# Kernel optimization log

Measured on AMD Instinct MI355X. Metric: run time of the kernel, lower is better.

The kernel has to match this reference:

```python
import jax, jax.numpy as jnp
import numpy as np
from jax.scipy.special import logsumexp

VOCAB = 50000; CHAR_VOCAB = 100
B, S, LC = 32, 256, 16
WDIM, CDIM, CNN_OUT, POS, ENR = 256, 124, 32, 36, 7
H = 512
T = 18  # num_classes + 1
IN0 = WDIM + POS + CNN_OUT + ENR  # 331
IN1 = 2 * H


def setup_inputs() -> dict:
    ks = jax.random.split(jax.random.key(0), 40)
    p = lambda i, shape: jax.random.normal(ks[i], shape, jnp.float32) * 0.05
    inp = {
        "x_word": jax.random.randint(ks[0], (B, S), 0, VOCAB),
        "x_pos": jax.random.normal(ks[1], (B, S, POS), jnp.float32),
        "x_char": jax.random.randint(ks[2], (B, S, LC), 0, CHAR_VOCAB),
        "x_enrich": jax.random.normal(ks[3], (B, S, ENR), jnp.float32),
        "mask": jnp.ones((B, S), jnp.bool_),
        "y_word": jax.random.randint(ks[4], (B, S), 0, T),
        "word_embed_W": p(5, (VOCAB, WDIM)),
        "char_embed_W": p(6, (CHAR_VOCAB, CDIM)),
        "cnn_W": p(7, (CNN_OUT, CDIM, 5)),
        "cnn_b": p(8, (CNN_OUT,)),
        "lin1_W": p(9, (128, IN1)), "lin1_b": p(10, (128,)),
        "lin2_W": p(11, (T, 128)), "lin2_b": p(12, (T,)),
        "crf_start": p(13, (T,)), "crf_end": p(14, (T,)), "crf_trans": p(15, (T, T)),
    }
    for j, (nm, din) in enumerate([("l0f", IN0), ("l0b", IN0), ("l1f", IN1), ("l1b", IN1)]):
        inp[nm + "_Wih"] = p(16 + 3 * j, (4 * H, din))
        inp[nm + "_Whh"] = p(17 + 3 * j, (4 * H, H))
        inp[nm + "_b"] = p(18 + 3 * j, (4 * H,))
    return inp


def _lstm_dir(xT, Wih, Whh, b, reverse):
    # xT: [S, B, D]; PyTorch gate order i, f, g, o; bias = b_ih + b_hh folded.
    Bn, Hn = xT.shape[1], Whh.shape[1]
    def step(carry, xt):
        h, c = carry
        z = xt @ Wih.T + h @ Whh.T + b
        i, f, g, o = jnp.split(z, 4, axis=-1)
        c2 = jax.nn.sigmoid(f) * c + jax.nn.sigmoid(i) * jnp.tanh(g)
        h2 = jax.nn.sigmoid(o) * jnp.tanh(c2)
        return (h2, c2), h2
    z0 = jnp.zeros((Bn, Hn), xT.dtype)
    _, hs = jax.lax.scan(step, (z0, z0), xT, reverse=reverse)
    return hs  # [S, B, H]


def _bilstm(x, prm):
    # x: [B, S, D]; prm: 4 tuples (Wih, Whh, b) = layer0 fwd/bwd, layer1 fwd/bwd
    xT = jnp.swapaxes(x, 0, 1)
    h = jnp.concatenate([_lstm_dir(xT, *prm[0], False), _lstm_dir(xT, *prm[1], True)], -1)
    h = jnp.concatenate([_lstm_dir(h, *prm[2], False), _lstm_dir(h, *prm[3], True)], -1)
    return jnp.swapaxes(h, 0, 1)  # [B, S, 2H]


def _emissions(x_word, x_pos, x_char, x_enrich, word_embed_W, char_embed_W,
               cnn_W, cnn_b, prm, lin1_W, lin1_b, lin2_W, lin2_b):
    Bn, Sn = x_word.shape
    we = word_embed_W[x_word]                               # [B, S, WDIM]
    ce = char_embed_W[x_char]                               # [B, S, LC, CDIM]
    ce = ce.reshape(Bn * Sn, LC, CDIM).transpose(0, 2, 1)   # [B*S, CDIM, LC]
    conv = jax.lax.conv_general_dilated(
        ce, cnn_W, (1,), 'VALID', dimension_numbers=('NCH', 'OIH', 'NCH')
    ) + cnn_b[None, :, None]                                # [B*S, CNN_OUT, LC-4]
    cpool = conv.max(-1).reshape(Bn, Sn, CNN_OUT)           # global max pool
    x = jax.nn.relu(jnp.concatenate([we, x_pos, cpool, x_enrich], -1))  # [B, S, 331]
    h = _bilstm(x, prm)                                     # [B, S, 1024]
    h1 = h @ lin1_W.T + lin1_b                              # [B, S, 128] (no activation)
    return h1 @ lin2_W.T + lin2_b                           # [B, S, T]


def _crf_nll(em, tags, mask, start, end, trans):
    # pytorch-crf: -llh with reduction='token_mean'
    m = mask.astype(em.dtype)
    em_sc = jnp.take_along_axis(em, tags[..., None], 2)[..., 0]        # [B, S]
    tr_sc = trans[tags[:, :-1], tags[:, 1:]]                           # [B, S-1]
    num = start[tags[:, 0]] + em_sc[:, 0] + jnp.sum(m[:, 1:] * (tr_sc + em_sc[:, 1:]), 1)
    seq_len = mask.sum(1).astype(jnp.int32)
    last_tag = jnp.take_along_axis(tags, (seq_len - 1)[:, None], 1)[:, 0]
    num = num + end[last_tag]
    score = start[None] + em[:, 0]                                     # [B, T]
    def step(sc, inp):
        e_t, m_t = inp
        nxt = logsumexp(sc[:, :, None] + trans[None] + e_t[:, None, :], axis=1)
        return jnp.where(m_t[:, None], nxt, sc), None
    score, _ = jax.lax.scan(step, score,
                            (jnp.swapaxes(em[:, 1:], 0, 1), jnp.swapaxes(mask[:, 1:], 0, 1)))
    logZ = logsumexp(score + end[None], -1)
    return -(num - logZ).sum() / m.sum()


def _viterbi(em, start, end, trans):
    # decode() is called without mask -> all timesteps valid
    score = start[None] + em[:, 0]                                     # [B, T]
    def step(sc, e_t):
        cand = sc[:, :, None] + trans[None]                            # [B, T, T]
        return jnp.max(cand, 1) + e_t, jnp.argmax(cand, 1)
    score, hist = jax.lax.scan(step, score, jnp.swapaxes(em[:, 1:], 0, 1))  # hist: [S-1, B, T]
    last = jnp.argmax(score + end[None], -1)                           # [B]
    def back(tag, idx_t):
        prev = jnp.take_along_axis(idx_t, tag[:, None], 1)[:, 0]
        return prev, prev
    _, prevs = jax.lax.scan(back, last, hist, reverse=True)            # [S-1, B]
    return jnp.concatenate([prevs, last[None]], 0).T                   # [B, S]


def reference(x_word, x_pos, x_char, x_enrich, mask, y_word,
              word_embed_W, char_embed_W, cnn_W, cnn_b,
              lin1_W, lin1_b, lin2_W, lin2_b,
              crf_start, crf_end, crf_trans,
              l0f_Wih, l0f_Whh, l0f_b, l0b_Wih, l0b_Whh, l0b_b,
              l1f_Wih, l1f_Whh, l1f_b, l1b_Wih, l1b_Whh, l1b_b):
    prm = [(l0f_Wih, l0f_Whh, l0f_b), (l0b_Wih, l0b_Whh, l0b_b),
           (l1f_Wih, l1f_Whh, l1f_b), (l1b_Wih, l1b_Whh, l1b_b)]
    em = _emissions(x_word, x_pos, x_char, x_enrich, word_embed_W, char_embed_W,
                    cnn_W, cnn_b, prm, lin1_W, lin1_b, lin2_W, lin2_b)
    decoded = _viterbi(em, crf_start, crf_end, crf_trans)
    loss = _crf_nll(em, y_word, mask, crf_start, crf_end, crf_trans)
    return em, decoded, loss
```

## Files before the change

kernel.cpp:

```cpp
#include <hip/hip_runtime.h>
#include <hip/hip_bf16.h>
#include <math.h>

constexpr int NB   = 32;
constexpr int NS   = 256;
constexpr int NLC  = 16;
constexpr int NWD  = 256;
constexpr int NCD  = 124;
constexpr int NCO  = 32;
constexpr int NPOS = 36;
constexpr int NENR = 7;
constexpr int NH   = 512;
constexpr int NT   = 18;
constexpr int NIN0 = 331;
constexpr int NIN0P= 352;
constexpr int NIN1 = 1024;
constexpr int NBS  = NB*NS;
constexpr int NG4  = 4*NH;
constexpr int NGS  = 4096;
constexpr int NHID = 128;
constexpr int NCHUNK = 16;

typedef __attribute__((ext_vector_type(8))) short short8v;
typedef __attribute__((ext_vector_type(4))) float f32x4;
typedef __attribute__((address_space(3))) unsigned lds_u32;
typedef __attribute__((address_space(1))) const unsigned glb_u32;

__device__ __forceinline__ float sigmoidf_(float x){ return 1.0f/(1.0f+expf(-x)); }
__device__ __forceinline__ short f2bf(float f) {
    union { __hip_bfloat16 h; short s; } u;
    u.h = __float2bfloat16(f);
    return u.s;
}
__device__ __forceinline__ float bf2f(short s) {
    union { unsigned u; float f; } v;
    v.u = ((unsigned)(unsigned short)s) << 16;
    return v.f;
}
__device__ __forceinline__ unsigned packbf3(float v) {
    short hi = f2bf(v);
    short lo = f2bf(v - bf2f(hi));
    return ((unsigned)(unsigned short)hi << 16) | (unsigned short)lo;
}
__device__ __forceinline__ void unpack8(const unsigned* w, short8v& hi, short8v& lo) {
    union U { short8v s; unsigned u[4]; } H, L;
    #pragma unroll
    for (int i = 0; i < 4; i++) {
        H.u[i] = (w[2*i+1] & 0xFFFF0000u) | (w[2*i] >> 16);
        L.u[i] = (w[2*i+1] << 16) | (w[2*i] & 0xFFFFu);
    }
    hi = H.s; lo = L.s;
}
__device__ __forceinline__ unsigned ld_sc1(const unsigned* p) {
    return __hip_atomic_load(p, __ATOMIC_RELAXED, __HIP_MEMORY_SCOPE_AGENT);
}
__device__ __forceinline__ void st_sc1(unsigned* p, unsigned v) {
    __hip_atomic_store(p, v, __ATOMIC_RELAXED, __HIP_MEMORY_SCOPE_AGENT);
}

__global__ __launch_bounds__(128) void k_features(const int* __restrict__ x_word,
    const float* __restrict__ x_pos, const int* __restrict__ x_char,
    const float* __restrict__ x_enr, const float* __restrict__ wembW,
    const float* __restrict__ cembW, const float* __restrict__ cnnW,
    const float* __restrict__ cnnb,
    unsigned short* __restrict__ xh, unsigned short* __restrict__ xl)
{
    __shared__ float ce[NLC][NCD];
    __shared__ float wT[310*33];
    __shared__ float cv[NCO][14];
    __shared__ float cpool[NCO];
    int n = blockIdx.x;
    int tid = threadIdx.x;
    for (int i = tid; i < NLC*NCD; i += 128) {
        int l = i / NCD, c = i % NCD;
        ce[l][c] = cembW[x_char[n*NLC + l]*NCD + c];
    }
    float acc3[3] = {0.f, 0.f, 0.f};
    #pragma unroll
    for (int half = 0; half < 2; half++) {
        int csta = half*62;
        __syncthreads();
        for (int i = tid; i < 310*32; i += 128) {
            int o = i / 310, ck = i - o*310;
            wT[ck*33 + o] = cnnW[o*(NCD*5) + csta*5 + ck];
        }
        __syncthreads();
        #pragma unroll
        for (int q = 0; q < 3; q++) {
            int p = tid + q*128;
            int o = p & 31, t = p >> 5;
            float acc = acc3[q];
            for (int c = 0; c < 62; c++) {
                #pragma unroll
                for (int k = 0; k < 5; k++)
                    acc += ce[t+k][csta + c] * wT[(c*5+k)*33 + o];
            }
            acc3[q] = acc;
        }
    }
    #pragma unroll
    for (int q = 0; q < 3; q++) {
        int p = tid + q*128;
        cv[p & 31][p >> 5] = acc3[q];
    }
    __syncthreads();
    if (tid < NCO) {
        float m = cv[tid][0];
        #pragma unroll
        for (int t = 1; t < 12; t++) m = fmaxf(m, cv[tid][t]);
        cpool[tid] = m + cnnb[tid];
    }
    __syncthreads();
    int widx = x_word[n];
    for (int j = tid; j < NIN0P; j += 128) {
        float v;
        if (j < NWD)            v = wembW[(size_t)widx*NWD + j];
        else if (j < NWD+NPOS)  v = x_pos[n*NPOS + (j-NWD)];
        else if (j < NWD+NPOS+NCO) v = cpool[j-(NWD+NPOS)];
        else if (j < NIN0)      v = x_enr[n*NENR + (j-(NWD+NPOS+NCO))];
        else                    v = 0.f;
        v = fmaxf(v, 0.f);
        short hi = f2bf(v);
        xh[(size_t)n*NIN0P + j] = (unsigned short)hi;
        xl[(size_t)n*NIN0P + j] = (unsigned short)f2bf(v - bf2f(hi));
    }
}

__global__ void k_pack_w(const float* __restrict__ W,
                         unsigned short* __restrict__ Wh, unsigned short* __restrict__ Wl,
                         int N, int Ksrc, int Kdst)
{
    int idx = blockIdx.x*256 + threadIdx.x;
    if (idx >= N*Kdst) return;
    int n = idx / Kdst, k = idx % Kdst;
    float v = (k < Ksrc) ? W[(size_t)n*Ksrc + k] : 0.f;
    short hi = f2bf(v);
    Wh[idx] = (unsigned short)hi;
    Wl[idx] = (unsigned short)f2bf(v - bf2f(hi));
}

constexpr int HBK = 32;
__global__ __launch_bounds__(256, 2) void k_gemm_hl(
    const unsigned short* __restrict__ Ah, const unsigned short* __restrict__ Al,
    const unsigned short* __restrict__ Bh, const unsigned short* __restrict__ Bl,
    const float* __restrict__ bias, float* __restrict__ C,
    int M, int N, int K)
{
    __shared__ unsigned short sA[2][2][128*HBK];
    __shared__ unsigned short sB[2][2][128*HBK];
    int bx = blockIdx.x, by = blockIdx.y;
    {
        int nMb = gridDim.x, nNb = gridDim.y;
        if (((nMb | nNb) & 3) == 0) {
            int lin = by * nMb + bx;
            int sid = lin >> 4, rem = lin & 15;
            int spr = nNb >> 2;
            int sm = sid / spr, sn = sid - sm*spr;
            bx = sm*4 + (rem >> 2);
            by = sn*4 + (rem & 3);
        }
    }
    int bm = bx*128, bn = by*128;
    int tid = threadIdx.x;
    int l = tid & 63, wv = tid >> 6;
    int wm = wv >> 1, wn = wv & 1;
    int lr = l & 15, lk = l >> 4;

    const unsigned short* gplane = (wv == 0) ? Ah : (wv == 1) ? Al : (wv == 2) ? Bh : Bl;
    int gbase = (wv < 2) ? bm : bn;
    unsigned short* lplane0 = (wv == 0) ? sA[0][0] : (wv == 1) ? sA[0][1]
                           : (wv == 2) ? sB[0][0] : sB[0][1];
    unsigned short* lplane1 = (wv == 0) ? sA[1][0] : (wv == 1) ? sA[1][1]
                           : (wv == 2) ? sB[1][0] : sB[1][1];
    int lrow = l >> 2;
    int gu = (l & 3);

    auto stage = [&](int kt, int buf) {
        unsigned short* lp0 = buf ? lplane1 : lplane0;
        #pragma unroll
        for (int rr = 0; rr < 8; rr++) {
            int row = rr*16 + lrow;
            int guS = gu ^ (row & 3);
            glb_u32* gp = (glb_u32*)(gplane + (size_t)(gbase + row)*K + (size_t)kt*HBK + guS*8);
            lds_u32* lp = (lds_u32*)(lp0 + (rr*16)*HBK);
            __builtin_amdgcn_global_load_lds(gp, lp, 16, 0, 0);
        }
    };

    f32x4 acc[4][4];
    #pragma unroll
    for (int i = 0; i < 4; i++)
        #pragma unroll
        for (int j = 0; j < 4; j++) acc[i][j] = (f32x4){0.f,0.f,0.f,0.f};

    int KT = K / HBK;
    stage(0, 0);
    int cur = 0;
    for (int kt = 0; kt < KT; kt++) {
        __syncthreads();
        if (kt+1 < KT) stage(kt+1, cur^1);
        short8v fAh[4], fAl[4], fBh[4], fBl[4];
        #pragma unroll
        for (int f = 0; f < 4; f++) {
            int ra = wm*64 + f*16 + lr, ua = (lk ^ (ra & 3))*8;
            fAh[f] = *(const short8v*)&sA[cur][0][ra*HBK + ua];
            fAl[f] = *(const short8v*)&sA[cur][1][ra*HBK + ua];
            int rb = wn*64 + f*16 + lr, ub = (lk ^ (rb & 3))*8;
            fBh[f] = *(const short8v*)&sB[cur][0][rb*HBK + ub];
            fBl[f] = *(const short8v*)&sB[cur][1][rb*HBK + ub];
        }
        #pragma unroll
        for (int i = 0; i < 4; i++)
            #pragma unroll
            for (int j = 0; j < 4; j++) {
                acc[i][j] = __builtin_amdgcn_mfma_f32_16x16x32_bf16(fAh[i], fBh[j], acc[i][j], 0, 0, 0);
                acc[i][j] = __builtin_amdgcn_mfma_f32_16x16x32_bf16(fAl[i], fBh[j], acc[i][j], 0, 0, 0);
                acc[i][j] = __builtin_amdgcn_mfma_f32_16x16x32_bf16(fAh[i], fBl[j], acc[i][j], 0, 0, 0);
            }
        cur ^= 1;
    }
    #pragma unroll
    for (int i = 0; i < 4; i++) {
        int m0 = bm + wm*64 + i*16 + lk*4;
        #pragma unroll
        for (int j = 0; j < 4; j++) {
            int n0 = bn + wn*64 + j*16 + lr;
            float bv = bias[n0];
            #pragma unroll
            for (int q = 0; q < 4; q++)
                C[(size_t)(m0+q)*N + n0] = acc[i][j][q] + bv;
        }
    }
}

__global__ __launch_bounds__(512, 2) void k_lstm_layer(
    const float* __restrict__ zxcat,
    const float* __restrict__ Whh_f, const float* __restrict__ Whh_b,
    unsigned short* __restrict__ h_hi, unsigned short* __restrict__ h_lo,
    unsigned* __restrict__ hbf, unsigned* __restrict__ flags)
{
    int chunk = blockIdx.x;
    int dir   = blockIdx.y;
    int tid = threadIdx.x;
    int wv = tid >> 6, l = tid & 63;
    int g  = wv & 3;
    int ks = wv >> 2;
    int lr = l & 15, lk = l >> 4;
    const float* zx  = zxcat + dir*NG4;
    const float* Whh = dir ? Whh_b : Whh_f;
    unsigned* hb = hbf + (size_t)dir * (2*NB*NH);
    unsigned* flag = flags + (size_t)dir * NCHUNK * 16;

    short8v bwh[2][8], bwl[2][8];
    #pragma unroll
    for (int uh = 0; uh < 2; uh++) {
        const float* wrow = Whh + ((size_t)(g*NH + chunk*32 + uh*16 + lr))*NH + ks*256 + lk*8;
        #pragma unroll
        for (int kt = 0; kt < 8; kt++) {
            float u[8];
            *(float4*)&u[0] = *(const float4*)(wrow + kt*32);
            *(float4*)&u[4] = *(const float4*)(wrow + kt*32 + 4);
            short8v sh, sl;
            #pragma unroll
            for (int j = 0; j < 8; j++) {
                short hi = f2bf(u[j]);
                sh[j] = hi;
                sl[j] = f2bf(u[j] - bf2f(hi));
            }
            bwh[uh][kt] = sh; bwl[uh][kt] = sl;
        }
    }

    __shared__ unsigned hstage[32*516];
    __shared__ float zsh[2][4][32][33];
    float c0 = 0.f, c1 = 0.f;

    for (int t = 0; t < NS; t++) {
        int t_eff = dir ? (NS-1-t) : t;

        float pz[2][4];
        #pragma unroll
        for (int cc = 0; cc < 2; cc++) {
            int cell = tid + cc*512, b = cell >> 5, u = cell & 31;
            const float* zr = zx + ((size_t)(b*NS + t_eff))*NGS + chunk*32 + u;
            #pragma unroll
            for (int g2 = 0; g2 < 4; g2++) pz[cc][g2] = zr[g2*NH];
        }

        if (t > 0) {
            {
                const unsigned* fp = &flag[(l & 15)*16];
                unsigned v;
                do { v = ld_sc1(fp); } while (!__all((int)(v >= (unsigned)t)));
                asm volatile("" ::: "memory");
            }
            const unsigned* hp = hb + ((t-1)&1)*(NB*NH);
            unsigned sv[32];
            #pragma unroll
            for (int i = 0; i < 32; i++) sv[i] = ld_sc1(hp + i*512 + tid);
            #pragma unroll
            for (int i = 0; i < 32; i++) hstage[i*516 + tid] = sv[i];
        }
        __syncthreads();

        f32x4 acc[2][2][3];
        #pragma unroll
        for (int bh = 0; bh < 2; bh++)
            #pragma unroll
            for (int uh = 0; uh < 2; uh++)
                #pragma unroll
                for (int q = 0; q < 3; q++) acc[bh][uh][q] = (f32x4){0.f,0.f,0.f,0.f};
        if (t > 0) {
            #pragma unroll
            for (int kt = 0; kt < 8; kt++) {
                short8v ah[2], al[2];
                #pragma unroll
                for (int bh = 0; bh < 2; bh++) {
                    unsigned w8[8];
                    const unsigned* sp = hstage + (bh*16+lr)*516 + ks*256 + kt*32 + lk*8;
                    *(uint4*)&w8[0] = *(const uint4*)sp;
                    *(uint4*)&w8[4] = *(const uint4*)(sp+4);
                    unpack8(w8, ah[bh], al[bh]);
                }
                #pragma unroll
                for (int bh = 0; bh < 2; bh++)
                    #pragma unroll
                    for (int uh = 0; uh < 2; uh++) {
                        acc[bh][uh][0] = __builtin_amdgcn_mfma_f32_16x16x32_bf16(ah[bh], bwh[uh][kt], acc[bh][uh][0], 0, 0, 0);
                        acc[bh][uh][1] = __builtin_amdgcn_mfma_f32_16x16x32_bf16(al[bh], bwh[uh][kt], acc[bh][uh][1], 0, 0, 0);
                        acc[bh][uh][2] = __builtin_amdgcn_mfma_f32_16x16x32_bf16(ah[bh], bwl[uh][kt], acc[bh][uh][2], 0, 0, 0);
                    }
            }
        }
        #pragma unroll
        for (int bh = 0; bh < 2; bh++)
            #pragma unroll
            for (int uh = 0; uh < 2; uh++)
                #pragma unroll
                for (int j = 0; j < 4; j++)
                    zsh[ks][g][bh*16 + lk*4 + j][uh*16 + lr] =
                        acc[bh][uh][0][j] + acc[bh][uh][1][j] + acc[bh][uh][2][j];
        __syncthreads();

        unsigned hq0 = 0, hq1 = 0;
        #pragma unroll
        for (int cc = 0; cc < 2; cc++) {
            int cell = tid + cc*512, b = cell >> 5, u = cell & 31;
            float zi = pz[cc][0] + zsh[0][0][b][u] + zsh[1][0][b][u];
            float zf = pz[cc][1] + zsh[0][1][b][u] + zsh[1][1][b][u];
            float zg = pz[cc][2] + zsh[0][2][b][u] + zsh[1][2][b][u];
            float zo = pz[cc][3] + zsh[0][3][b][u] + zsh[1][3][b][u];
            float cold = cc ? c1 : c0;
            float cn = sigmoidf_(zf)*cold + sigmoidf_(zi)*tanhf(zg);
            float hn = sigmoidf_(zo)*tanhf(cn);
            unsigned pk = packbf3(hn);
            if (cc) { c1 = cn; hq1 = pk; } else { c0 = cn; hq0 = pk; }
            st_sc1(&hb[(size_t)(t&1)*(NB*NH) + b*NH + chunk*32 + u], pk);
        }
        __syncthreads();
        if (tid == 0)
            st_sc1(&flag[chunk*16], (unsigned)(t+1));
        #pragma unroll
        for (int cc = 0; cc < 2; cc++) {
            int cell = tid + cc*512, b = cell >> 5, u = cell & 31;
            unsigned pk = cc ? hq1 : hq0;
            size_t o = ((size_t)(b*NS + t_eff))*NIN1 + dir*NH + chunk*32 + u;
            h_hi[o] = (unsigned short)(pk >> 16);
            h_lo[o] = (unsigned short)(pk & 0xFFFFu);
        }
    }
}

__global__ __launch_bounds__(256) void k_lin2(const float* __restrict__ hid,
    const float* __restrict__ W2, const float* __restrict__ b2, float* __restrict__ em)
{
    int flat = blockIdx.x*256 + threadIdx.x;
    if (flat >= NBS*NT) return;
    int m = flat / NT, j = flat % NT;
    const float* hr = hid + (size_t)m*NHID;
    const float* wr = W2 + j*NHID;
    float acc = b2[j];
    #pragma unroll 8
    for (int k = 0; k < NHID; k += 4) {
        float4 h4 = *(const float4*)(hr+k);
        float4 w4 = *(const float4*)(wr+k);
        acc += h4.x*w4.x + h4.y*w4.y + h4.z*w4.z + h4.w*w4.w;
    }
    em[flat] = acc;
}

__global__ __launch_bounds__(64) void k_crf(const float* __restrict__ em,
    const int* __restrict__ tags, const float* __restrict__ start,
    const float* __restrict__ endv, const float* __restrict__ trans,
    float* __restrict__ dec, float* __restrict__ partial)
{
    __shared__ float tr[NT][NT];
    __shared__ float vsc[NT], nsc[NT];
    __shared__ unsigned char hist[NS][NT];
    __shared__ float numsh;
    int b = blockIdx.x, tid = threadIdx.x;
    for (int i = tid; i < NT*NT; i += 64) tr[i/NT][i%NT] = trans[i];
    if (tid < NT) {
        float e0 = em[((size_t)b*NS)*NT + tid];
        vsc[tid] = start[tid] + e0;
        nsc[tid] = start[tid] + e0;
    }
    __syncthreads();
    const int* tg = tags + b*NS;
    float num = 0.f;
    for (int t = 1; t < NS; t++) {
        float nv_v = 0.f, nv_n = 0.f;
        if (tid < NT) {
            float emv = em[((size_t)b*NS + t)*NT + tid];
            float best = -1e30f; int bi = 0;
            float m = -1e30f;
            for (int i = 0; i < NT; i++) {
                float v = vsc[i] + tr[i][tid];
                if (v > best) { best = v; bi = i; }
                m = fmaxf(m, nsc[i] + tr[i][tid]);
            }
            hist[t][tid] = (unsigned char)bi;
            nv_v = best + emv;
            float s = 0.f;
            for (int i = 0; i < NT; i++) s += expf(nsc[i] + tr[i][tid] - m);
            nv_n = m + logf(s) + emv;
        } else if (tid == 32) {
            num += tr[tg[t-1]][tg[t]] + em[((size_t)b*NS + t)*NT + tg[t]];
        }
        __syncthreads();
        if (tid < NT) { vsc[tid] = nv_v; nsc[tid] = nv_n; }
        __syncthreads();
    }
    if (tid == 32) numsh = num;
    __syncthreads();
    if (tid == 0) {
        float bv = vsc[0] + endv[0]; int tag = 0;
        for (int j = 1; j < NT; j++) { float v = vsc[j] + endv[j]; if (v > bv) { bv = v; tag = j; } }
        dec[b*NS + NS-1] = (float)tag;
        for (int t = NS-1; t >= 1; t--) { tag = hist[t][tag]; dec[b*NS + t-1] = (float)tag; }
        float m = -1e30f;
        for (int j = 0; j < NT; j++) m = fmaxf(m, nsc[j] + endv[j]);
        float s = 0.f;
        for (int j = 0; j < NT; j++) s += expf(nsc[j] + endv[j] - m);
        float logZ = m + logf(s);
        float numer = start[tg[0]] + em[((size_t)b*NS)*NT + tg[0]] + numsh + endv[tg[NS-1]];
        partial[b] = -(numer - logZ);
    }
}

__global__ void k_loss_final(const float* __restrict__ partial, float* __restrict__ loss)
{
    if (threadIdx.x == 0 && blockIdx.x == 0) {
        float s = 0.f;
        for (int b = 0; b < NB; b++) s += partial[b];
        *loss = s / (float)(NB*NS);
    }
}

extern "C" void kernel_launch(void* const* d_in, const int* in_sizes, int n_in,
                              void* d_out, int out_size, void* d_ws, size_t ws_size,
                              hipStream_t stream)
{
    const int*   x_word = (const int*)d_in[0];
    const float* x_pos  = (const float*)d_in[1];
    const int*   x_char = (const int*)d_in[2];
    const float* x_enr  = (const float*)d_in[3];
    const int*   y_word = (const int*)d_in[5];
    const float* wembW  = (const float*)d_in[6];
    const float* cembW  = (const float*)d_in[7];
    const float* cnnW   = (const float*)d_in[8];
    const float* cnnb   = (const float*)d_in[9];
    const float* lin1W  = (const float*)d_in[10];
    const float* lin1b  = (const float*)d_in[11];
    const float* lin2W  = (const float*)d_in[12];
    const float* lin2b  = (const float*)d_in[13];
    const float* crf_s  = (const float*)d_in[14];
    const float* crf_e  = (const float*)d_in[15];
    const float* crf_tr = (const float*)d_in[16];
    const float* l0f_Wih = (const float*)d_in[17];
    const float* l0f_Whh = (const float*)d_in[18];
    const float* l0f_b   = (const float*)d_in[19];
    const float* l0b_Wih = (const float*)d_in[20];
    const float* l0b_Whh = (const float*)d_in[21];
    const float* l0b_b   = (const float*)d_in[22];
    const float* l1f_Wih = (const float*)d_in[23];
    const float* l1f_Whh = (const float*)d_in[24];
    const float* l1f_b   = (const float*)d_in[25];
    const float* l1b_Wih = (const float*)d_in[26];
    const float* l1b_Whh = (const float*)d_in[27];
    const float* l1b_b   = (const float*)d_in[28];

    char* wsb = (char*)d_ws;
    size_t off = 0;
    auto alloc = [&](size_t bytes) { char* p = wsb + off; off += (bytes + 255) & ~(size_t)255; return p; };
    unsigned short* xh  = (unsigned short*)alloc((size_t)NBS*NIN0P*2);
    unsigned short* xl  = (unsigned short*)alloc((size_t)NBS*NIN0P*2);
    unsigned short* w0h = (unsigned short*)alloc((size_t)NGS*NIN0P*2);
    unsigned short* w0l = (unsigned short*)alloc((size_t)NGS*NIN0P*2);
    unsigned short* w1h = (unsigned short*)alloc((size_t)NGS*NIN1*2);
    unsigned short* w1l = (unsigned short*)alloc((size_t)NGS*NIN1*2);
    unsigned short* wlh = (unsigned short*)alloc((size_t)NHID*NIN1*2);
    unsigned short* wll = (unsigned short*)alloc((size_t)NHID*NIN1*2);
    float*    zxcat = (float*)alloc((size_t)NBS*NGS*4);
    unsigned short* h0h = (unsigned short*)alloc((size_t)NBS*NIN1*2);
    unsigned short* h0l = (unsigned short*)alloc((size_t)NBS*NIN1*2);
    unsigned short* h1h = (unsigned short*)alloc((size_t)NBS*NIN1*2);
    unsigned short* h1l = (unsigned short*)alloc((size_t)NBS*NIN1*2);
    float*    hid1  = (float*)alloc((size_t)NBS*NHID*4);
    float*    partial = (float*)alloc(256);
    float*    bias0 = (float*)alloc((size_t)NGS*4);
    float*    bias1 = (float*)alloc((size_t)NGS*4);
    unsigned* hbf   = (unsigned*)alloc((size_t)2*2*NB*NH*4);
    unsigned* flags = (unsigned*)alloc((size_t)2*NCHUNK*16*4);

    float* em_out   = (float*)d_out;
    float* dec_out  = em_out + (size_t)NBS*NT;
    float* loss_out = dec_out + NBS;

    k_pack_w<<<(NG4*NIN0P+255)/256, 256, 0, stream>>>(l0f_Wih, w0h, w0l, NG4, NIN0, NIN0P);
    k_pack_w<<<(NG4*NIN0P+255)/256, 256, 0, stream>>>(l0b_Wih, w0h + (size_t)NG4*NIN0P, w0l + (size_t)NG4*NIN0P, NG4, NIN0, NIN0P);
    k_pack_w<<<(NG4*NIN1+255)/256, 256, 0, stream>>>(l1f_Wih, w1h, w1l, NG4, NIN1, NIN1);
    k_pack_w<<<(NG4*NIN1+255)/256, 256, 0, stream>>>(l1b_Wih, w1h + (size_t)NG4*NIN1, w1l + (size_t)NG4*NIN1, NG4, NIN1, NIN1);
    k_pack_w<<<(NHID*NIN1+255)/256, 256, 0, stream>>>(lin1W, wlh, wll, NHID, NIN1, NIN1);
    hipMemcpyAsync(bias0,       l0f_b, NG4*4, hipMemcpyDeviceToDevice, stream);
    hipMemcpyAsync(bias0 + NG4, l0b_b, NG4*4, hipMemcpyDeviceToDevice, stream);
    hipMemcpyAsync(bias1,       l1f_b, NG4*4, hipMemcpyDeviceToDevice, stream);
    hipMemcpyAsync(bias1 + NG4, l1b_b, NG4*4, hipMemcpyDeviceToDevice, stream);
    k_features<<<NBS, 128, 0, stream>>>(x_word, x_pos, x_char, x_enr, wembW, cembW, cnnW, cnnb, xh, xl);
    k_gemm_hl<<<dim3(NBS/128, NGS/128), 256, 0, stream>>>(xh, xl, w0h, w0l, bias0, zxcat, NBS, NGS, NIN0P);
    hipMemsetAsync(flags, 0, (size_t)2*NCHUNK*16*4, stream);
    k_lstm_layer<<<dim3(NCHUNK, 2), 512, 0, stream>>>(zxcat, l0f_Whh, l0b_Whh, h0h, h0l, hbf, flags);
    k_gemm_hl<<<dim3(NBS/128, NGS/128), 256, 0, stream>>>(h0h, h0l, w1h, w1l, bias1, zxcat, NBS, NGS, NIN1);
    hipMemsetAsync(flags, 0, (size_t)2*NCHUNK*16*4, stream);
    k_lstm_layer<<<dim3(NCHUNK, 2), 512, 0, stream>>>(zxcat, l1f_Whh, l1b_Whh, h1h, h1l, hbf, flags);
    k_gemm_hl<<<dim3(NBS/128, NHID/128), 256, 0, stream>>>(h1h, h1l, wlh, wll, lin1b, hid1, NBS, NHID, NIN1);
    k_lin2<<<(NBS*NT+255)/256, 256, 0, stream>>>(hid1, lin2W, lin2b, em_out);
    k_crf<<<NB, 64, 0, stream>>>(em_out, y_word, crf_s, crf_e, crf_tr, dec_out, partial);
    k_loss_final<<<1, 64, 0, stream>>>(partial, loss_out);
}
```

Measured before the change: 3.611 ms.

## Per-wave flags in LSTM recurrence, fuse head GEMMs, merge weight packing

Each wave in the LSTM recurrence now publishes its own progress flag after waiting only on its own outstanding stores, replacing the block-wide barrier before a single flag store. Consumers poll the per-wave flags with 64-bit loads. The lin1 GEMM and lin2 projection are fused into one kernel that keeps the hidden activations in LDS, and the five weight-packing launches become one. This cuts per-timestep synchronization latency and a few launches. It adds polling traffic and relies on the vmcnt wait to order the h stores before the flag.

```diff
diff --git a/kernel.cpp b/kernel.cpp
--- a/kernel.cpp
+++ b/kernel.cpp
@@ -21,6 +21,11 @@
 constexpr int NHID = 128;
 constexpr int NCHUNK = 16;
 
+constexpr int SW0 = NG4*NIN0P;
+constexpr int SW1 = NG4*NIN1;
+constexpr int SWL = NHID*NIN1;
+constexpr int SWTOT = 2*SW0 + 2*SW1 + SWL;
+
 typedef __attribute__((ext_vector_type(8))) short short8v;
 typedef __attribute__((ext_vector_type(4))) float f32x4;
 typedef __attribute__((address_space(3))) unsigned lds_u32;
@@ -53,6 +58,10 @@
 }
 __device__ __forceinline__ unsigned ld_sc1(const unsigned* p) {
     return __hip_atomic_load(p, __ATOMIC_RELAXED, __HIP_MEMORY_SCOPE_AGENT);
+}
+__device__ __forceinline__ unsigned long long ld64_sc1(const void* p) {
+    return __hip_atomic_load((const unsigned long long*)p, __ATOMIC_RELAXED,
+                             __HIP_MEMORY_SCOPE_AGENT);
 }
 __device__ __forceinline__ void st_sc1(unsigned* p, unsigned v) {
     __hip_atomic_store(p, v, __ATOMIC_RELAXED, __HIP_MEMORY_SCOPE_AGENT);
@@ -126,14 +135,27 @@
     }
 }
 
-__global__ void k_pack_w(const float* __restrict__ W,
-                         unsigned short* __restrict__ Wh, unsigned short* __restrict__ Wl,
-                         int N, int Ksrc, int Kdst)
+__global__ void k_pack_all(const float* __restrict__ W0f, const float* __restrict__ W0b,
+                           const float* __restrict__ W1f, const float* __restrict__ W1b,
+                           const float* __restrict__ WL,
+                           unsigned short* __restrict__ Wh, unsigned short* __restrict__ Wl)
 {
     int idx = blockIdx.x*256 + threadIdx.x;
-    if (idx >= N*Kdst) return;
-    int n = idx / Kdst, k = idx % Kdst;
-    float v = (k < Ksrc) ? W[(size_t)n*Ksrc + k] : 0.f;
+    if (idx >= SWTOT) return;
+    float v;
+    if (idx < 2*SW0) {
+        const float* src = (idx < SW0) ? W0f : W0b;
+        int loc = (idx < SW0) ? idx : idx - SW0;
+        int n = loc / NIN0P, k = loc - n*NIN0P;
+        v = (k < NIN0) ? src[(size_t)n*NIN0 + k] : 0.f;
+    } else if (idx < 2*SW0 + 2*SW1) {
+        int loc = idx - 2*SW0;
+        const float* src = (loc < SW1) ? W1f : W1b;
+        if (loc >= SW1) loc -= SW1;
+        v = src[loc];
+    } else {
+        v = WL[idx - (2*SW0 + 2*SW1)];
+    }
     short hi = f2bf(v);
     Wh[idx] = (unsigned short)hi;
     Wl[idx] = (unsigned short)f2bf(v - bf2f(hi));
@@ -233,6 +255,110 @@
     }
 }
 
+__global__ __launch_bounds__(256, 1) void k_gemm_head(
+    const unsigned short* __restrict__ Ah, const unsigned short* __restrict__ Al,
+    const unsigned short* __restrict__ Bh, const unsigned short* __restrict__ Bl,
+    const float* __restrict__ bias1, const float* __restrict__ W2,
+    const float* __restrict__ b2, float* __restrict__ em, int K)
+{
+    __shared__ unsigned short sA[2][2][128*HBK];
+    __shared__ unsigned short sB[2][2][128*HBK];
+    __shared__ float hidS[128*132];
+    __shared__ float w2S[NT*132];
+    __shared__ float b2S[NT];
+    int bm = blockIdx.x*128;
+    int tid = threadIdx.x;
+    int l = tid & 63, wv = tid >> 6;
+    int wm = wv >> 1, wn = wv & 1;
+    int lr = l & 15, lk = l >> 4;
+
+    for (int i = tid; i < NT*NHID; i += 256) {
+        int j = i >> 7, k = i & 127;
+        w2S[j*132 + k] = W2[i];
+    }
+    if (tid < NT) b2S[tid] = b2[tid];
+
+    const unsigned short* gplane = (wv == 0) ? Ah : (wv == 1) ? Al : (wv == 2) ? Bh : Bl;
+    int gbase = (wv < 2) ? bm : 0;
+    unsigned short* lplane0 = (wv == 0) ? sA[0][0] : (wv == 1) ? sA[0][1]
+                           : (wv == 2) ? sB[0][0] : sB[0][1];
+    unsigned short* lplane1 = (wv == 0) ? sA[1][0] : (wv == 1) ? sA[1][1]
+                           : (wv == 2) ? sB[1][0] : sB[1][1];
+    int lrow = l >> 2;
+    int gu = (l & 3);
+
+    auto stage = [&](int kt, int buf) {
+        unsigned short* lp0 = buf ? lplane1 : lplane0;
+        #pragma unroll
+        for (int rr = 0; rr < 8; rr++) {
+            int row = rr*16 + lrow;
+            int guS = gu ^ (row & 3);
+            glb_u32* gp = (glb_u32*)(gplane + (size_t)(gbase + row)*K + (size_t)kt*HBK + guS*8);
+            lds_u32* lp = (lds_u32*)(lp0 + (rr*16)*HBK);
+            __builtin_amdgcn_global_load_lds(gp, lp, 16, 0, 0);
+        }
+    };
+
+    f32x4 acc[4][4];
+    #pragma unroll
+    for (int i = 0; i < 4; i++)
+        #pragma unroll
+        for (int j = 0; j < 4; j++) acc[i][j] = (f32x4){0.f,0.f,0.f,0.f};
+
+    int KT = K / HBK;
+    stage(0, 0);
+    int cur = 0;
+    for (int kt = 0; kt < KT; kt++) {
+        __syncthreads();
+        if (kt+1 < KT) stage(kt+1, cur^1);
+        short8v fAh[4], fAl[4], fBh[4], fBl[4];
+        #pragma unroll
+        for (int f = 0; f < 4; f++) {
+            int ra = wm*64 + f*16 + lr, ua = (lk ^ (ra & 3))*8;
+            fAh[f] = *(const short8v*)&sA[cur][0][ra*HBK + ua];
+            fAl[f] = *(const short8v*)&sA[cur][1][ra*HBK + ua];
+            int rb = wn*64 + f*16 + lr, ub = (lk ^ (rb & 3))*8;
+            fBh[f] = *(const short8v*)&sB[cur][0][rb*HBK + ub];
+            fBl[f] = *(const short8v*)&sB[cur][1][rb*HBK + ub];
+        }
+        #pragma unroll
+        for (int i = 0; i < 4; i++)
+            #pragma unroll
+            for (int j = 0; j < 4; j++) {
+                acc[i][j] = __builtin_amdgcn_mfma_f32_16x16x32_bf16(fAh[i], fBh[j], acc[i][j], 0, 0, 0);
+                acc[i][j] = __builtin_amdgcn_mfma_f32_16x16x32_bf16(fAl[i], fBh[j], acc[i][j], 0, 0, 0);
+                acc[i][j] = __builtin_amdgcn_mfma_f32_16x16x32_bf16(fAh[i], fBl[j], acc[i][j], 0, 0, 0);
+            }
+        cur ^= 1;
+    }
+    #pragma unroll
+    for (int i = 0; i < 4; i++) {
+        int mloc = wm*64 + i*16 + lk*4;
+        #pragma unroll
+        for (int j = 0; j < 4; j++) {
+            int nloc = wn*64 + j*16 + lr;
+            float bv = bias1[nloc];
+            #pragma unroll
+            for (int q = 0; q < 4; q++)
+                hidS[(mloc+q)*132 + nloc] = acc[i][j][q] + bv;
+        }
+    }
+    __syncthreads();
+    for (int oi = tid; oi < 128*NT; oi += 256) {
+        int m = oi / NT, j = oi - m*NT;
+        const float* hr = &hidS[m*132];
+        const float* wr = &w2S[j*132];
+        float s = b2S[j];
+        #pragma unroll 8
+        for (int k = 0; k < NHID; k += 4) {
+            float4 h4 = *(const float4*)(hr+k);
+            float4 w4 = *(const float4*)(wr+k);
+            s += h4.x*w4.x + h4.y*w4.y + h4.z*w4.z + h4.w*w4.w;
+        }
+        em[(size_t)(bm+m)*NT + j] = s;
+    }
+}
+
 __global__ __launch_bounds__(512, 2) void k_lstm_layer(
     const float* __restrict__ zxcat,
     const float* __restrict__ Whh_f, const float* __restrict__ Whh_b,
@@ -249,7 +375,7 @@
     const float* zx  = zxcat + dir*NG4;
     const float* Whh = dir ? Whh_b : Whh_f;
     unsigned* hb = hbf + (size_t)dir * (2*NB*NH);
-    unsigned* flag = flags + (size_t)dir * NCHUNK * 16;
+    unsigned* flag = flags + (size_t)dir * (NCHUNK*8);
 
     short8v bwh[2][8], bwl[2][8];
     #pragma unroll
@@ -289,9 +415,11 @@
 
         if (t > 0) {
             {
-                const unsigned* fp = &flag[(l & 15)*16];
-                unsigned v;
-                do { v = ld_sc1(fp); } while (!__all((int)(v >= (unsigned)t)));
+                const unsigned long long* fp = (const unsigned long long*)flag + l;
+                unsigned tv = (unsigned)t;
+                unsigned long long v;
+                do { v = ld64_sc1(fp); }
+                while (!__all(((unsigned)v >= tv) && ((unsigned)(v>>32) >= tv)));
                 asm volatile("" ::: "memory");
             }
             const unsigned* hp = hb + ((t-1)&1)*(NB*NH);
@@ -357,9 +485,8 @@
             if (cc) { c1 = cn; hq1 = pk; } else { c0 = cn; hq0 = pk; }
             st_sc1(&hb[(size_t)(t&1)*(NB*NH) + b*NH + chunk*32 + u], pk);
         }
-        __syncthreads();
-        if (tid == 0)
-            st_sc1(&flag[chunk*16], (unsigned)(t+1));
+        asm volatile("s_waitcnt vmcnt(0)" ::: "memory");
+        if (l == 0) st_sc1(&flag[chunk*8 + wv], (unsigned)(t+1));
         #pragma unroll
         for (int cc = 0; cc < 2; cc++) {
             int cell = tid + cc*512, b = cell >> 5, u = cell & 31;
@@ -369,24 +496,6 @@
             h_lo[o] = (unsigned short)(pk & 0xFFFFu);
         }
     }
-}
-
-__global__ __launch_bounds__(256) void k_lin2(const float* __restrict__ hid,
-    const float* __restrict__ W2, const float* __restrict__ b2, float* __restrict__ em)
-{
-    int flat = blockIdx.x*256 + threadIdx.x;
-    if (flat >= NBS*NT) return;
-    int m = flat / NT, j = flat % NT;
-    const float* hr = hid + (size_t)m*NHID;
-    const float* wr = W2 + j*NHID;
-    float acc = b2[j];
-    #pragma unroll 8
-    for (int k = 0; k < NHID; k += 4) {
-        float4 h4 = *(const float4*)(hr+k);
-        float4 w4 = *(const float4*)(wr+k);
-        acc += h4.x*w4.x + h4.y*w4.y + h4.z*w4.z + h4.w*w4.w;
-    }
-    em[flat] = acc;
 }
 
 __global__ __launch_bounds__(64) void k_crf(const float* __restrict__ em,
@@ -495,46 +604,44 @@
     auto alloc = [&](size_t bytes) { char* p = wsb + off; off += (bytes + 255) & ~(size_t)255; return p; };
     unsigned short* xh  = (unsigned short*)alloc((size_t)NBS*NIN0P*2);
     unsigned short* xl  = (unsigned short*)alloc((size_t)NBS*NIN0P*2);
-    unsigned short* w0h = (unsigned short*)alloc((size_t)NGS*NIN0P*2);
-    unsigned short* w0l = (unsigned short*)alloc((size_t)NGS*NIN0P*2);
-    unsigned short* w1h = (unsigned short*)alloc((size_t)NGS*NIN1*2);
-    unsigned short* w1l = (unsigned short*)alloc((size_t)NGS*NIN1*2);
-    unsigned short* wlh = (unsigned short*)alloc((size_t)NHID*NIN1*2);
-    unsigned short* wll = (unsigned short*)alloc((size_t)NHID*NIN1*2);
+    unsigned short* whA = (unsigned short*)alloc((size_t)SWTOT*2);
+    unsigned short* wlA = (unsigned short*)alloc((size_t)SWTOT*2);
     float*    zxcat = (float*)alloc((size_t)NBS*NGS*4);
     unsigned short* h0h = (unsigned short*)alloc((size_t)NBS*NIN1*2);
     unsigned short* h0l = (unsigned short*)alloc((size_t)NBS*NIN1*2);
     unsigned short* h1h = (unsigned short*)alloc((size_t)NBS*NIN1*2);
     unsigned short* h1l = (unsigned short*)alloc((size_t)NBS*NIN1*2);
-    float*    hid1  = (float*)alloc((size_t)NBS*NHID*4);
     float*    partial = (float*)alloc(256);
     float*    bias0 = (float*)alloc((size_t)NGS*4);
     float*    bias1 = (float*)alloc((size_t)NGS*4);
     unsigned* hbf   = (unsigned*)alloc((size_t)2*2*NB*NH*4);
-    unsigned* flags = (unsigned*)alloc((size_t)2*NCHUNK*16*4);
+    unsigned* flags = (unsigned*)alloc((size_t)2*NCHUNK*8*4);
+
+    unsigned short* w0h = whA;
+    unsigned short* w1h = whA + 2*(size_t)SW0;
+    unsigned short* wlh = whA + 2*(size_t)SW0 + 2*(size_t)SW1;
+    unsigned short* w0l = wlA;
+    unsigned short* w1l = wlA + 2*(size_t)SW0;
+    unsigned short* wll = wlA + 2*(size_t)SW0 + 2*(size_t)SW1;
 
     float* em_out   = (float*)d_out;
     float* dec_out  = em_out + (size_t)NBS*NT;
     float* loss_out = dec_out + NBS;
 
-    k_pack_w<<<(NG4*NIN0P+255)/256, 256, 0, stream>>>(l0f_Wih, w0h, w0l, NG4, NIN0, NIN0P);
-    k_pack_w<<<(NG4*NIN0P+255)/256, 256, 0, stream>>>(l0b_Wih, w0h + (size_t)NG4*NIN0P, w0l + (size_t)NG4*NIN0P, NG4, NIN0, NIN0P);
-    k_pack_w<<<(NG4*NIN1+255)/256, 256, 0, stream>>>(l1f_Wih, w1h, w1l, NG4, NIN1, NIN1);
-    k_pack_w<<<(NG4*NIN1+255)/256, 256, 0, stream>>>(l1b_Wih, w1h + (size_t)NG4*NIN1, w1l + (size_t)NG4*NIN1, NG4, NIN1, NIN1);
-    k_pack_w<<<(NHID*NIN1+255)/256, 256, 0, stream>>>(lin1W, wlh, wll, NHID, NIN1, NIN1);
+    k_pack_all<<<(SWTOT+255)/256, 256, 0, stream>>>(l0f_Wih, l0b_Wih, l1f_Wih, l1b_Wih,
+                                                    lin1W, whA, wlA);
     hipMemcpyAsync(bias0,       l0f_b, NG4*4, hipMemcpyDeviceToDevice, stream);
     hipMemcpyAsync(bias0 + NG4, l0b_b, NG4*4, hipMemcpyDeviceToDevice, stream);
     hipMemcpyAsync(bias1,       l1f_b, NG4*4, hipMemcpyDeviceToDevice, stream);
     hipMemcpyAsync(bias1 + NG4, l1b_b, NG4*4, hipMemcpyDeviceToDevice, stream);
     k_features<<<NBS, 128, 0, stream>>>(x_word, x_pos, x_char, x_enr, wembW, cembW, cnnW, cnnb, xh, xl);
     k_gemm_hl<<<dim3(NBS/128, NGS/128), 256, 0, stream>>>(xh, xl, w0h, w0l, bias0, zxcat, NBS, NGS, NIN0P);
-    hipMemsetAsync(flags, 0, (size_t)2*NCHUNK*16*4, stream);
+    hipMemsetAsync(flags, 0, (size_t)2*NCHUNK*8*4, stream);
     k_lstm_layer<<<dim3(NCHUNK, 2), 512, 0, stream>>>(zxcat, l0f_Whh, l0b_Whh, h0h, h0l, hbf, flags);
     k_gemm_hl<<<dim3(NBS/128, NGS/128), 256, 0, stream>>>(h0h, h0l, w1h, w1l, bias1, zxcat, NBS, NGS, NIN1);
-    hipMemsetAsync(flags, 0, (size_t)2*NCHUNK*16*4, stream);
+    hipMemsetAsync(flags, 0, (size_t)2*NCHUNK*8*4, stream);
     k_lstm_layer<<<dim3(NCHUNK, 2), 512, 0, stream>>>(zxcat, l1f_Whh, l1b_Whh, h1h, h1l, hbf, flags);
-    k_gemm_hl<<<dim3(NBS/128, NHID/128), 256, 0, stream>>>(h1h, h1l, wlh, wll, lin1b, hid1, NBS, NHID, NIN1);
-    k_lin2<<<(NBS*NT+255)/256, 256, 0, stream>>>(hid1, lin2W, lin2b, em_out);
+    k_gemm_head<<<NBS/128, 256, 0, stream>>>(h1h, h1l, wlh, wll, lin1b, lin2W, lin2b, em_out, NIN1);
     k_crf<<<NB, 64, 0, stream>>>(em_out, y_word, crf_s, crf_e, crf_tr, dec_out, partial);
     k_loss_final<<<1, 64, 0, stream>>>(partial, loss_out);
 }
```

Result: slower. 4.960 ms (+37.4%).
